# Performance work log

Hardware: AMD Instinct MI355X
Metric: run time of the kernel (lower is better)

Reference implementation:

```python
import jax, jax.numpy as jnp
import numpy as np

EPS = 1e-09

def setup_inputs() -> dict:
    key = jax.random.key(0)
    k1, k2 = jax.random.split(key)
    bs, n1, n2, d = 2048, 4, 4, 4608
    input1 = jax.random.uniform(k1, (bs, n1, d), dtype=jnp.float32)
    input2 = jax.random.uniform(k2, (bs, n2, d), dtype=jnp.float32)
    mask1 = jnp.ones((bs, n1, d), dtype=jnp.float32)
    mask2 = jnp.ones((bs, n2, d), dtype=jnp.float32)
    return {"input1": input1, "mask1": mask1, "input2": input2, "mask2": mask2}

def reference(input1, mask1, input2, mask2) -> jnp.ndarray:
    # p: (bs, n1, d), q: (bs, n2, d)
    p = input1 * mask1
    q = input2 * mask2
    # KL(p_i || q_j) = sum_d p_i * (log(p_i+eps) - log(q_j+eps))
    # decomposed: per-row entropy-like term minus a batched matmul,
    # avoiding the (bs, n1, n2, d) broadcast intermediate.
    ent = jnp.sum(p * jnp.log(p + EPS), axis=-1)          # (bs, n1)
    cross = jnp.einsum('bid,bjd->bij', p, jnp.log(q + EPS))  # (bs, n1, n2)
    div = ent[:, :, None] - cross                          # (bs, n1, n2)
    return -div
```

## Files before the change

### kernel.cpp

```cpp
#include <hip/hip_runtime.h>


constexpr int   D   = 4608;
constexpr int   DV  = D / 4;
constexpr int   NT  = 256;
constexpr float EPS = 1e-9f;

__global__ __launch_bounds__(NT)
void nkld_kernel(const float* __restrict__ in1, const float* __restrict__ m1,
                 const float* __restrict__ in2, const float* __restrict__ m2,
                 float* __restrict__ out)
{
    const int b   = blockIdx.x;
    const int tid = threadIdx.x;

    const size_t base = (size_t)b * 4 * D;
    const float4* p1 = reinterpret_cast<const float4*>(in1 + base);
    const float4* g1 = reinterpret_cast<const float4*>(m1  + base);
    const float4* p2 = reinterpret_cast<const float4*>(in2 + base);
    const float4* g2 = reinterpret_cast<const float4*>(m2  + base);

    float ent[4]      = {0.f, 0.f, 0.f, 0.f};
    float cross[4][4] = {{0.f,0.f,0.f,0.f},{0.f,0.f,0.f,0.f},
                         {0.f,0.f,0.f,0.f},{0.f,0.f,0.f,0.f}};

    for (int v = tid; v < DV; v += NT) {
        float4 pv[4];
        float4 lq[4];
        #pragma unroll
        for (int i = 0; i < 4; ++i) {
            float4 a  = p1[(size_t)i * DV + v];
            float4 ma = g1[(size_t)i * DV + v];
            float4 p  = make_float4(a.x * ma.x, a.y * ma.y, a.z * ma.z, a.w * ma.w);
            pv[i] = p;
            ent[i] += p.x * __logf(p.x + EPS);
            ent[i] += p.y * __logf(p.y + EPS);
            ent[i] += p.z * __logf(p.z + EPS);
            ent[i] += p.w * __logf(p.w + EPS);
        }
        #pragma unroll
        for (int j = 0; j < 4; ++j) {
            float4 c  = p2[(size_t)j * DV + v];
            float4 mc = g2[(size_t)j * DV + v];
            lq[j] = make_float4(__logf(c.x * mc.x + EPS),
                                __logf(c.y * mc.y + EPS),
                                __logf(c.z * mc.z + EPS),
                                __logf(c.w * mc.w + EPS));
        }
        #pragma unroll
        for (int i = 0; i < 4; ++i) {
            #pragma unroll
            for (int j = 0; j < 4; ++j) {
                cross[i][j] += pv[i].x * lq[j].x + pv[i].y * lq[j].y
                             + pv[i].z * lq[j].z + pv[i].w * lq[j].w;
            }
        }
    }

    float vals[20];
    #pragma unroll
    for (int i = 0; i < 4; ++i) vals[i] = ent[i];
    #pragma unroll
    for (int i = 0; i < 4; ++i)
        #pragma unroll
        for (int j = 0; j < 4; ++j) vals[4 + i * 4 + j] = cross[i][j];

    #pragma unroll
    for (int off = 32; off > 0; off >>= 1) {
        #pragma unroll
        for (int k = 0; k < 20; ++k)
            vals[k] += __shfl_down(vals[k], off, 64);
    }

    __shared__ float red[4][20];
    const int wave = tid >> 6;
    const int lane = tid & 63;
    if (lane == 0) {
        #pragma unroll
        for (int k = 0; k < 20; ++k) red[wave][k] = vals[k];
    }
    __syncthreads();

    if (tid < 16) {
        const int i = tid >> 2;
        float c = 0.f, e = 0.f;
        #pragma unroll
        for (int w = 0; w < 4; ++w) {
            c += red[w][4 + tid];
            e += red[w][i];
        }
        out[(size_t)b * 16 + tid] = c - e;
    }
}

extern "C" void kernel_launch(void* const* d_in, const int* in_sizes, int n_in,
                              void* d_out, int out_size, void* d_ws, size_t ws_size,
                              hipStream_t stream) {
    const float* in1 = (const float*)d_in[0];
    const float* m1  = (const float*)d_in[1];
    const float* in2 = (const float*)d_in[2];
    const float* m2  = (const float*)d_in[3];
    float* out = (float*)d_out;
    nkld_kernel<<<dim3(2048), dim3(NT), 0, stream>>>(in1, m1, in2, m2, out);
}
```

Baseline: 485.9 us.

## Assign one q row per wave with double-buffered loads and split entropy

Each wave now owns one q row j and walks the full D range itself, computing log(q_j) once per element and dotting it with all four p rows. The entropy work is also split so that wave j computes only ent[j]. Loads are double-buffered in registers across two strided chunks, and the cross-wave reduction shrinks from 20 values to 5 per wave. The cost is that every wave re-reads all four p rows (four times the p traffic, which should mostly hit L2 or cache). There is also a larger register footprint, with launch bounds set for occupancy 4.

Measured after the change: 545.7 us. 12.3% more time.

```diff
diff --git a/kernel.cpp b/kernel.cpp
--- a/kernel.cpp
+++ b/kernel.cpp
@@ -6,90 +6,120 @@
 constexpr int   NT  = 256;
 constexpr float EPS = 1e-9f;
 
-__global__ __launch_bounds__(NT)
+struct Buf {
+    float4 c, mc, a0, ma0, a1, ma1, a2, ma2, a3, ma3;
+};
+
+__device__ __forceinline__ void load10(Buf& B,
+        const float4* __restrict__ p1, const float4* __restrict__ g1,
+        const float4* __restrict__ q2, const float4* __restrict__ g2, int v)
+{
+    B.c   = q2[v];
+    B.mc  = g2[v];
+    B.a0  = p1[v];
+    B.ma0 = g1[v];
+    B.a1  = p1[v + DV];
+    B.ma1 = g1[v + DV];
+    B.a2  = p1[v + 2 * DV];
+    B.ma2 = g1[v + 2 * DV];
+    B.a3  = p1[v + 3 * DV];
+    B.ma3 = g1[v + 3 * DV];
+}
+
+__device__ __forceinline__ float4 mul4(float4 a, float4 b) {
+    return make_float4(a.x * b.x, a.y * b.y, a.z * b.z, a.w * b.w);
+}
+__device__ __forceinline__ float4 log4e(float4 a) {
+    return make_float4(__logf(a.x + EPS), __logf(a.y + EPS),
+                       __logf(a.z + EPS), __logf(a.w + EPS));
+}
+__device__ __forceinline__ float dot4(float4 a, float4 b) {
+    return a.x * b.x + a.y * b.y + a.z * b.z + a.w * b.w;
+}
+
+template<int J>
+__device__ __forceinline__ void computeB(const Buf& B, float* cr, float& ent)
+{
+    float4 lq = log4e(mul4(B.c, B.mc));
+    float4 p0 = mul4(B.a0, B.ma0);
+    float4 p1 = mul4(B.a1, B.ma1);
+    float4 p2 = mul4(B.a2, B.ma2);
+    float4 p3 = mul4(B.a3, B.ma3);
+    cr[0] += dot4(p0, lq);
+    cr[1] += dot4(p1, lq);
+    cr[2] += dot4(p2, lq);
+    cr[3] += dot4(p3, lq);
+    const float4 pj = (J == 0) ? p0 : (J == 1) ? p1 : (J == 2) ? p2 : p3;
+    ent += dot4(pj, log4e(pj));
+}
+
+template<int J>
+__device__ __forceinline__ void waveBody(
+        const float4* __restrict__ p1, const float4* __restrict__ g1,
+        const float4* __restrict__ q2, const float4* __restrict__ g2,
+        int lane, float* cr, float& ent)
+{
+    Buf A, B;
+    int v = lane;
+    load10(A, p1, g1, q2, g2, v);
+    for (int k = 0; k < 18; k += 2) {
+        load10(B, p1, g1, q2, g2, v + 64);
+        computeB<J>(A, cr, ent);
+        if (k + 2 < 18) load10(A, p1, g1, q2, g2, v + 128);
+        computeB<J>(B, cr, ent);
+        v += 128;
+    }
+}
+
+__global__ __launch_bounds__(NT, 4)
 void nkld_kernel(const float* __restrict__ in1, const float* __restrict__ m1,
                  const float* __restrict__ in2, const float* __restrict__ m2,
                  float* __restrict__ out)
 {
-    const int b   = blockIdx.x;
-    const int tid = threadIdx.x;
+    const int b    = blockIdx.x;
+    const int tid  = threadIdx.x;
+    const int wave = tid >> 6;
+    const int lane = tid & 63;
 
     const size_t base = (size_t)b * 4 * D;
     const float4* p1 = reinterpret_cast<const float4*>(in1 + base);
     const float4* g1 = reinterpret_cast<const float4*>(m1  + base);
-    const float4* p2 = reinterpret_cast<const float4*>(in2 + base);
-    const float4* g2 = reinterpret_cast<const float4*>(m2  + base);
+    const float4* q2 = reinterpret_cast<const float4*>(in2 + base) + (size_t)wave * DV;
+    const float4* g2 = reinterpret_cast<const float4*>(m2  + base) + (size_t)wave * DV;
 
-    float ent[4]      = {0.f, 0.f, 0.f, 0.f};
-    float cross[4][4] = {{0.f,0.f,0.f,0.f},{0.f,0.f,0.f,0.f},
-                         {0.f,0.f,0.f,0.f},{0.f,0.f,0.f,0.f}};
+    float cr[4] = {0.f, 0.f, 0.f, 0.f};
+    float ent = 0.f;
 
-    for (int v = tid; v < DV; v += NT) {
-        float4 pv[4];
-        float4 lq[4];
-        #pragma unroll
-        for (int i = 0; i < 4; ++i) {
-            float4 a  = p1[(size_t)i * DV + v];
-            float4 ma = g1[(size_t)i * DV + v];
-            float4 p  = make_float4(a.x * ma.x, a.y * ma.y, a.z * ma.z, a.w * ma.w);
-            pv[i] = p;
-            ent[i] += p.x * __logf(p.x + EPS);
-            ent[i] += p.y * __logf(p.y + EPS);
-            ent[i] += p.z * __logf(p.z + EPS);
-            ent[i] += p.w * __logf(p.w + EPS);
-        }
-        #pragma unroll
-        for (int j = 0; j < 4; ++j) {
-            float4 c  = p2[(size_t)j * DV + v];
-            float4 mc = g2[(size_t)j * DV + v];
-            lq[j] = make_float4(__logf(c.x * mc.x + EPS),
-                                __logf(c.y * mc.y + EPS),
-                                __logf(c.z * mc.z + EPS),
-                                __logf(c.w * mc.w + EPS));
-        }
-        #pragma unroll
-        for (int i = 0; i < 4; ++i) {
-            #pragma unroll
-            for (int j = 0; j < 4; ++j) {
-                cross[i][j] += pv[i].x * lq[j].x + pv[i].y * lq[j].y
-                             + pv[i].z * lq[j].z + pv[i].w * lq[j].w;
-            }
-        }
+    switch (wave) {
+        case 0: waveBody<0>(p1, g1, q2, g2, lane, cr, ent); break;
+        case 1: waveBody<1>(p1, g1, q2, g2, lane, cr, ent); break;
+        case 2: waveBody<2>(p1, g1, q2, g2, lane, cr, ent); break;
+        case 3: waveBody<3>(p1, g1, q2, g2, lane, cr, ent); break;
     }
-
-    float vals[20];
-    #pragma unroll
-    for (int i = 0; i < 4; ++i) vals[i] = ent[i];
-    #pragma unroll
-    for (int i = 0; i < 4; ++i)
-        #pragma unroll
-        for (int j = 0; j < 4; ++j) vals[4 + i * 4 + j] = cross[i][j];
 
     #pragma unroll
     for (int off = 32; off > 0; off >>= 1) {
-        #pragma unroll
-        for (int k = 0; k < 20; ++k)
-            vals[k] += __shfl_down(vals[k], off, 64);
+        cr[0] += __shfl_down(cr[0], off, 64);
+        cr[1] += __shfl_down(cr[1], off, 64);
+        cr[2] += __shfl_down(cr[2], off, 64);
+        cr[3] += __shfl_down(cr[3], off, 64);
+        ent   += __shfl_down(ent,   off, 64);
     }
 
-    __shared__ float red[4][20];
-    const int wave = tid >> 6;
-    const int lane = tid & 63;
+    __shared__ float ent_s[4];
+    __shared__ float cr_s[4][4];
     if (lane == 0) {
-        #pragma unroll
-        for (int k = 0; k < 20; ++k) red[wave][k] = vals[k];
+        ent_s[wave]   = ent;
+        cr_s[wave][0] = cr[0];
+        cr_s[wave][1] = cr[1];
+        cr_s[wave][2] = cr[2];
+        cr_s[wave][3] = cr[3];
     }
     __syncthreads();
 
     if (tid < 16) {
-        const int i = tid >> 2;
-        float c = 0.f, e = 0.f;
-        #pragma unroll
-        for (int w = 0; w < 4; ++w) {
-            c += red[w][4 + tid];
-            e += red[w][i];
-        }
-        out[(size_t)b * 16 + tid] = c - e;
+        const int i = tid >> 2, j = tid & 3;
+        out[(size_t)b * 16 + tid] = cr_s[j][i] - ent_s[i];
     }
 }
 
```

## Double-buffer input chunks into LDS via global_load_lds and share log(q) across waves

Applied to the files above, without the earlier changes.

Rewrites the main loop so each block streams 64-column chunks of all four inputs straight into a double-buffered LDS area with the global_load_lds builtin, prefetching the next chunk while computing the current one. Each wave now owns one p row. log(q) is computed once per chunk into shared memory and reused by all four waves. The per-thread reduction shrinks from 20 accumulators to 5. The goal is more memory traffic in flight and less register pressure in this bandwidth-bound kernel. In exchange it adds two barriers per chunk and about 36KB of LDS per block, which may limit occupancy.

Measured after the change: 473.5 us. -2.5%, faster.

```diff
diff --git a/kernel.cpp b/kernel.cpp
--- a/kernel.cpp
+++ b/kernel.cpp
@@ -1,105 +1,113 @@
 #include <hip/hip_runtime.h>
+#include <stdint.h>
 
 
-constexpr int   D   = 4608;
-constexpr int   DV  = D / 4;
 constexpr int   NT  = 256;
 constexpr float EPS = 1e-9f;
 
+__device__ __forceinline__ float4 mul4(float4 a, float4 b) {
+    return make_float4(a.x*b.x, a.y*b.y, a.z*b.z, a.w*b.w);
+}
+__device__ __forceinline__ float4 log4e(float4 a) {
+    return make_float4(__logf(a.x+EPS), __logf(a.y+EPS),
+                       __logf(a.z+EPS), __logf(a.w+EPS));
+}
+__device__ __forceinline__ float dot4(float4 a, float4 b) {
+    return a.x*b.x + a.y*b.y + a.z*b.z + a.w*b.w;
+}
+
+__device__ __forceinline__ void gll16(const float4* g, float4* l) {
+    __builtin_amdgcn_global_load_lds(
+        (const __attribute__((address_space(1))) uint32_t*)(const void*)g,
+        (__attribute__((address_space(3))) uint32_t*)(void*)l,
+        16 , 0, 0);
+}
+
 __global__ __launch_bounds__(NT)
-void nkld_kernel(const float* __restrict__ in1, const float* __restrict__ m1,
-                 const float* __restrict__ in2, const float* __restrict__ m2,
+void nkld_kernel(const float4* __restrict__ A0, const float4* __restrict__ A1,
+                 const float4* __restrict__ A2, const float4* __restrict__ A3,
                  float* __restrict__ out)
 {
-    const int b   = blockIdx.x;
-    const int tid = threadIdx.x;
+    __shared__ float4 buf[2][1024];
+    __shared__ float4 slq[256];
+    __shared__ float  ent_s[4];
+    __shared__ float  cr_s[4][4];
 
-    const size_t base = (size_t)b * 4 * D;
-    const float4* p1 = reinterpret_cast<const float4*>(in1 + base);
-    const float4* g1 = reinterpret_cast<const float4*>(m1  + base);
-    const float4* p2 = reinterpret_cast<const float4*>(in2 + base);
-    const float4* g2 = reinterpret_cast<const float4*>(m2  + base);
+    const int b    = blockIdx.x;
+    const int tid  = threadIdx.x;
+    const int w    = tid >> 6;
+    const int lane = tid & 63;
+    const int soff = b * 4608 + w * 1152 + lane;
 
-    float ent[4]      = {0.f, 0.f, 0.f, 0.f};
-    float cross[4][4] = {{0.f,0.f,0.f,0.f},{0.f,0.f,0.f,0.f},
-                         {0.f,0.f,0.f,0.f},{0.f,0.f,0.f,0.f}};
+    float cr0=0.f, cr1=0.f, cr2=0.f, cr3=0.f, ent=0.f;
 
-    for (int v = tid; v < DV; v += NT) {
-        float4 pv[4];
-        float4 lq[4];
-        #pragma unroll
-        for (int i = 0; i < 4; ++i) {
-            float4 a  = p1[(size_t)i * DV + v];
-            float4 ma = g1[(size_t)i * DV + v];
-            float4 p  = make_float4(a.x * ma.x, a.y * ma.y, a.z * ma.z, a.w * ma.w);
-            pv[i] = p;
-            ent[i] += p.x * __logf(p.x + EPS);
-            ent[i] += p.y * __logf(p.y + EPS);
-            ent[i] += p.z * __logf(p.z + EPS);
-            ent[i] += p.w * __logf(p.w + EPS);
+    gll16(A0 + soff, &buf[0][tid]);
+    gll16(A1 + soff, &buf[0][256 + tid]);
+    gll16(A2 + soff, &buf[0][512 + tid]);
+    gll16(A3 + soff, &buf[0][768 + tid]);
+    asm volatile("s_waitcnt vmcnt(0)" ::: "memory");
+    __builtin_amdgcn_s_barrier();
+
+    int cur = 0;
+    #pragma unroll 1
+    for (int c = 0; c < 18; ++c) {
+        if (c + 1 < 18) {
+            const int o = soff + (c + 1) * 64;
+            float4* dst = buf[cur ^ 1];
+            gll16(A0 + o, dst + tid);
+            gll16(A1 + o, dst + 256 + tid);
+            gll16(A2 + o, dst + 512 + tid);
+            gll16(A3 + o, dst + 768 + tid);
         }
-        #pragma unroll
-        for (int j = 0; j < 4; ++j) {
-            float4 c  = p2[(size_t)j * DV + v];
-            float4 mc = g2[(size_t)j * DV + v];
-            lq[j] = make_float4(__logf(c.x * mc.x + EPS),
-                                __logf(c.y * mc.y + EPS),
-                                __logf(c.z * mc.z + EPS),
-                                __logf(c.w * mc.w + EPS));
+        {
+            float4 q  = buf[cur][512 + tid];
+            float4 mq = buf[cur][768 + tid];
+            slq[tid] = log4e(mul4(q, mq));
         }
-        #pragma unroll
-        for (int i = 0; i < 4; ++i) {
-            #pragma unroll
-            for (int j = 0; j < 4; ++j) {
-                cross[i][j] += pv[i].x * lq[j].x + pv[i].y * lq[j].y
-                             + pv[i].z * lq[j].z + pv[i].w * lq[j].w;
-            }
+        asm volatile("s_waitcnt lgkmcnt(0)" ::: "memory");
+        __builtin_amdgcn_s_barrier();
+        {
+            float4 p = mul4(buf[cur][w*64 + lane], buf[cur][256 + w*64 + lane]);
+            ent += dot4(p, log4e(p));
+            cr0 += dot4(p, slq[lane]);
+            cr1 += dot4(p, slq[ 64 + lane]);
+            cr2 += dot4(p, slq[128 + lane]);
+            cr3 += dot4(p, slq[192 + lane]);
         }
+        asm volatile("s_waitcnt vmcnt(0) lgkmcnt(0)" ::: "memory");
+        __builtin_amdgcn_s_barrier();
+        cur ^= 1;
     }
-
-    float vals[20];
-    #pragma unroll
-    for (int i = 0; i < 4; ++i) vals[i] = ent[i];
-    #pragma unroll
-    for (int i = 0; i < 4; ++i)
-        #pragma unroll
-        for (int j = 0; j < 4; ++j) vals[4 + i * 4 + j] = cross[i][j];
 
     #pragma unroll
     for (int off = 32; off > 0; off >>= 1) {
-        #pragma unroll
-        for (int k = 0; k < 20; ++k)
-            vals[k] += __shfl_down(vals[k], off, 64);
+        cr0 += __shfl_down(cr0, off, 64);
+        cr1 += __shfl_down(cr1, off, 64);
+        cr2 += __shfl_down(cr2, off, 64);
+        cr3 += __shfl_down(cr3, off, 64);
+        ent += __shfl_down(ent, off, 64);
     }
-
-    __shared__ float red[4][20];
-    const int wave = tid >> 6;
-    const int lane = tid & 63;
     if (lane == 0) {
-        #pragma unroll
-        for (int k = 0; k < 20; ++k) red[wave][k] = vals[k];
+        ent_s[w]   = ent;
+        cr_s[w][0] = cr0;
+        cr_s[w][1] = cr1;
+        cr_s[w][2] = cr2;
+        cr_s[w][3] = cr3;
     }
     __syncthreads();
-
     if (tid < 16) {
-        const int i = tid >> 2;
-        float c = 0.f, e = 0.f;
-        #pragma unroll
-        for (int w = 0; w < 4; ++w) {
-            c += red[w][4 + tid];
-            e += red[w][i];
-        }
-        out[(size_t)b * 16 + tid] = c - e;
+        const int i = tid >> 2, j = tid & 3;
+        out[(size_t)b * 16 + tid] = cr_s[i][j] - ent_s[i];
     }
 }
 
 extern "C" void kernel_launch(void* const* d_in, const int* in_sizes, int n_in,
                               void* d_out, int out_size, void* d_ws, size_t ws_size,
                               hipStream_t stream) {
-    const float* in1 = (const float*)d_in[0];
-    const float* m1  = (const float*)d_in[1];
-    const float* in2 = (const float*)d_in[2];
-    const float* m2  = (const float*)d_in[3];
+    const float4* A0 = (const float4*)d_in[0];
+    const float4* A1 = (const float4*)d_in[1];
+    const float4* A2 = (const float4*)d_in[2];
+    const float4* A3 = (const float4*)d_in[3];
     float* out = (float*)d_out;
-    nkld_kernel<<<dim3(2048), dim3(NT), 0, stream>>>(in1, m1, in2, m2, out);
+    nkld_kernel<<<dim3(2048), dim3(NT), 0, stream>>>(A0, A1, A2, A3, out);
 }
```
